# Performance work log

Measured on AMD Instinct MI355X. Metric: run time of the kernel, lower is better.

## Reference

```python
import jax, jax.numpy as jnp
import numpy as np

B, N, E = 16, 10000, 160000
C_IN, C_SP, C_OUT = 32, 16, 32


def _glorot(key, shape):
    s = float(np.sqrt(6.0 / (shape[0] + shape[1])))
    return jax.random.uniform(key, shape, jnp.float32, -s, s)


def setup_inputs() -> dict:
    key = jax.random.key(0)
    ks = jax.random.split(key, 12)
    X = jax.random.normal(ks[0], (B, N, C_IN), jnp.float32)
    edge_index1 = jax.random.randint(ks[1], (2, E), 0, N)
    edge_weight1 = jax.random.uniform(ks[2], (E,), jnp.float32)
    res_n_id1 = jnp.arange(N)
    edge_index2 = jax.random.randint(ks[3], (2, E), 0, N)
    edge_weight2 = jax.random.uniform(ks[4], (E,), jnp.float32)
    res_n_id2 = jnp.arange(N)
    # conv1 params (in=C_IN, out=C_SP, edge_channels=1, concat=True)
    amp_w1 = _glorot(ks[5], (1, C_IN))            # [edge_ch, in]
    gate_w1 = _glorot(ks[6], (2 * C_IN + 1, 1))   # Linear(2*in+edge_ch, 1)
    gate_b1 = jnp.zeros((1,), jnp.float32)
    w1 = _glorot(ks[7], (2 * C_IN, C_SP))         # concat weight
    b1 = jnp.zeros((C_SP,), jnp.float32)
    # conv2 params (in=C_SP, out=C_OUT)
    amp_w2 = _glorot(ks[8], (1, C_SP))
    gate_w2 = _glorot(ks[9], (2 * C_SP + 1, 1))
    gate_b2 = jnp.zeros((1,), jnp.float32)
    w2 = _glorot(ks[10], (2 * C_SP, C_OUT))
    b2 = jnp.zeros((C_OUT,), jnp.float32)
    return dict(X=X, edge_index1=edge_index1, edge_weight1=edge_weight1, res_n_id1=res_n_id1,
                edge_index2=edge_index2, edge_weight2=edge_weight2, res_n_id2=res_n_id2,
                amp_w1=amp_w1, gate_w1=gate_w1, gate_b1=gate_b1, w1=w1, b1=b1,
                amp_w2=amp_w2, gate_w2=gate_w2, gate_b2=gate_b2, w2=w2, b2=b2)


def _sagela(x_src, x_dst, edge_index, edge_weight, amp_w, gate_w, gate_b, w, b):
    # x_src: [B, N_src, C], x_dst: [B, N_dst, C]
    src, dst = edge_index[0], edge_index[1]
    n_dst = x_dst.shape[1]
    C = x_src.shape[-1]
    x_j = x_src[:, src]                       # [B, E, C] gathered source feats
    x_i = x_dst[:, dst]                       # [B, E, C] gathered target feats
    e = edge_weight[:, None]                  # [E, 1] edge features
    # gate_linear(cat[x_i, x_j, e]) split into three matmuls (same math)
    wg_i, wg_j, wg_e = gate_w[:C], gate_w[C:2 * C], gate_w[2 * C:]
    lamb = jax.nn.sigmoid(x_i @ wg_i + x_j @ wg_j + (e @ wg_e)[None] + gate_b)  # [B, E, 1]
    amp = e @ amp_w                           # [E, C] edge amplification
    msg = amp[None, :, :] * x_j * lamb        # [B, E, C]
    # mean aggregation over incoming edges (scatter-add / count)
    aggr = jnp.zeros((x_src.shape[0], n_dst, C), msg.dtype).at[:, dst].add(msg)
    cnt = jnp.zeros((n_dst,), msg.dtype).at[dst].add(1.0)
    aggr = aggr / jnp.maximum(cnt, 1.0)[None, :, None]
    out = jnp.concatenate([x_dst, aggr], axis=-1) @ w + b  # [B, N_dst, out]
    return out


def reference(X, edge_index1, edge_weight1, res_n_id1, edge_index2, edge_weight2, res_n_id2,
              amp_w1, gate_w1, gate_b1, w1, b1, amp_w2, gate_w2, gate_b2, w2, b2):
    h = _sagela(X, X[:, res_n_id1], edge_index1, edge_weight1, amp_w1, gate_w1, gate_b1, w1, b1)
    h = jax.nn.leaky_relu(h, 0.01)
    out = _sagela(h, h[:, res_n_id2], edge_index2, edge_weight2, amp_w2, gate_w2, gate_b2, w2, b2)
    return out
```

## Files before the change

kernel.cpp:

```cpp
#include <hip/hip_runtime.h>
#include <math.h>

#define B 16
#define N 10000
#define E 160000
#define CAP 64

__device__ __forceinline__ ushort f2bf(float v) {
    uint u = __float_as_uint(v);
    u = (u + 0x7fffu + ((u >> 16) & 1u)) >> 16;
    return (ushort)u;
}
__device__ __forceinline__ float bf2f(ushort u) { return __uint_as_float(((uint)u) << 16); }
__device__ __forceinline__ float bf2f_lo(uint u) { return __uint_as_float(u << 16); }
__device__ __forceinline__ float bf2f_hi(uint u) { return __uint_as_float(u & 0xffff0000u); }
__device__ __forceinline__ float dec_ew(uint u) {
    return ((float)(u >> 14) + 0.5f) * (1.0f / 262144.0f);
}

__global__ __launch_bounds__(256, 8)
void prep_fused_kernel(const float* __restrict__ X,
                       const float* __restrict__ gate_w1,
                       const float* __restrict__ amp_w1,
                       const float* __restrict__ b1,
                       const int* __restrict__ ei1, const float* __restrict__ ew1,
                       const int* __restrict__ ei2, const float* __restrict__ ew2,
                       const float* __restrict__ w1,
                       ushort* __restrict__ yt,
                       float* __restrict__ xpart,
                       float* __restrict__ gi, float* __restrict__ gj,
                       int* __restrict__ bcount1, uint* __restrict__ bucket1,
                       int* __restrict__ bcount2, uint* __restrict__ bucket2) {
    __shared__ __align__(16) float s_w1[64 * 16];
    __shared__ float s_x[16][33];
    __shared__ float s_py[16][17];

    int tid = threadIdx.x;
    int gtid = blockIdx.x * 256 + tid;

    if (gtid < 2 * E) {
        if (gtid < E) {
            int t = gtid;
            int d = ei1[E + t];
            int pos = atomicAdd(&bcount1[d], 1);
            if (pos < CAP) {
                uint q = (uint)(ew1[t] * 262144.0f);
                if (q > 262143u) q = 262143u;
                bucket1[d * CAP + pos] = (q << 14) | (uint)ei1[t];
            }
        } else {
            int e = gtid - E;
            int d = ei2[E + e];
            int pos = atomicAdd(&bcount2[d], 1);
            if (pos < CAP) {
                uint q = (uint)(ew2[e] * 262144.0f);
                if (q > 262143u) q = 262143u;
                bucket2[d * CAP + pos] = (q << 14) | (uint)ei2[e];
            }
        }
    }

    {
        int i = tid * 4;
        *(float4*)&s_w1[i] = *(const float4*)&w1[i];
    }
    int b = tid >> 4, o = tid & 15;
    for (int n = blockIdx.x; n < N; n += gridDim.x) {
        __syncthreads();
        {
            int bb = tid >> 4, c2 = (tid & 15) * 2;
            float2 v = *(const float2*)(X + ((size_t)bb * N + n) * 32 + c2);
            s_x[bb][c2] = v.x; s_x[bb][c2 + 1] = v.y;
        }
        __syncthreads();

        float po = b1[o], py = 0.f;
        #pragma unroll
        for (int c = 0; c < 32; ++c) {
            float xa = s_x[b][c];
            po += xa * s_w1[c * 16 + o];
            py += amp_w1[c] * xa * s_w1[(32 + c) * 16 + o];
        }
        float pi = s_x[b][o] * gate_w1[o]      + s_x[b][o + 16] * gate_w1[o + 16];
        float pj = s_x[b][o] * gate_w1[32 + o] + s_x[b][o + 16] * gate_w1[48 + o];
        #pragma unroll
        for (int off = 8; off; off >>= 1) {
            pi += __shfl_xor(pi, off, 16);
            pj += __shfl_xor(pj, off, 16);
        }
        int r = n * 16 + b;
        xpart[(size_t)r * 16 + o] = po;
        s_py[b][o] = py;
        if (o == 0) { gi[r] = pi; gj[r] = pj; }
        __syncthreads();

        if (tid < 64) {
            int bb = tid >> 2, j = tid & 3;
            uint lo = (uint)f2bf(s_py[bb][4 * j])     | ((uint)f2bf(s_py[bb][4 * j + 1]) << 16);
            uint hi = (uint)f2bf(s_py[bb][4 * j + 2]) | ((uint)f2bf(s_py[bb][4 * j + 3]) << 16);
            ((uint2*)yt)[(size_t)(n * 16 + bb) * 4 + j] = make_uint2(lo, hi);
        }
    }
}

__global__ __launch_bounds__(256, 8)
void agg1_kernel(const uint4* __restrict__ y4,
                 const float* __restrict__ xpart,
                 const float* __restrict__ gi,
                 const float* __restrict__ gj,
                 const int* __restrict__ bcount,
                 const uint* __restrict__ bucket,
                 const float* __restrict__ gate_w,
                 const float* __restrict__ gate_b,
                 const float* __restrict__ gate_w2,
                 ushort* __restrict__ htb,
                 float* __restrict__ gi2, float* __restrict__ gj2) {
    int tid = threadIdx.x;
    int wv = tid >> 6, l = tid & 63;
    int n = blockIdx.x * 4 + wv;
    int og = l & 1, b = (l >> 1) & 15, h = l >> 5;

    int cnt = bcount[n];
    int deg = cnt < CAP ? cnt : CAP;
    float wge = gate_w[64];
    float gib = gi[n * 16 + b] + gate_b[0];
    const uint* __restrict__ eb = bucket + (size_t)n * CAP;

    float a0 = 0.f, a1 = 0.f, a2 = 0.f, a3 = 0.f;
    float a4 = 0.f, a5 = 0.f, a6 = 0.f, a7 = 0.f;
    for (int k = h; k < deg; k += 2) {
        uint pr = eb[k];
        uint src = pr & 0x3FFFu;
        float w = dec_ew(pr);
        float z = gib + gj[src * 16 + b] + w * wge;
        float cc = w / (1.0f + __expf(-z));
        uint4 u = y4[src * 32u + (uint)b * 2u + og];
        a0 += cc * bf2f_lo(u.x); a1 += cc * bf2f_hi(u.x);
        a2 += cc * bf2f_lo(u.y); a3 += cc * bf2f_hi(u.y);
        a4 += cc * bf2f_lo(u.z); a5 += cc * bf2f_hi(u.z);
        a6 += cc * bf2f_lo(u.w); a7 += cc * bf2f_hi(u.w);
    }
    a0 += __shfl_xor(a0, 32, 64); a1 += __shfl_xor(a1, 32, 64);
    a2 += __shfl_xor(a2, 32, 64); a3 += __shfl_xor(a3, 32, 64);
    a4 += __shfl_xor(a4, 32, 64); a5 += __shfl_xor(a5, 32, 64);
    a6 += __shfl_xor(a6, 32, 64); a7 += __shfl_xor(a7, 32, 64);

    if (h == 0) {
        float inv = 1.0f / fmaxf((float)cnt, 1.0f);
        size_t xb = ((size_t)n * 16 + b) * 16 + 8 * og;
        float4 xp0 = *(const float4*)&xpart[xb];
        float4 xp1 = *(const float4*)&xpart[xb + 4];
        float v0 = xp0.x + inv * a0, v1 = xp0.y + inv * a1;
        float v2 = xp0.z + inv * a2, v3 = xp0.w + inv * a3;
        float v4 = xp1.x + inv * a4, v5 = xp1.y + inv * a5;
        float v6 = xp1.z + inv * a6, v7 = xp1.w + inv * a7;
        v0 = v0 > 0.f ? v0 : 0.01f * v0;  v1 = v1 > 0.f ? v1 : 0.01f * v1;
        v2 = v2 > 0.f ? v2 : 0.01f * v2;  v3 = v3 > 0.f ? v3 : 0.01f * v3;
        v4 = v4 > 0.f ? v4 : 0.01f * v4;  v5 = v5 > 0.f ? v5 : 0.01f * v5;
        v6 = v6 > 0.f ? v6 : 0.01f * v6;  v7 = v7 > 0.f ? v7 : 0.01f * v7;
        uint4 pk;
        pk.x = (uint)f2bf(v0) | ((uint)f2bf(v1) << 16);
        pk.y = (uint)f2bf(v2) | ((uint)f2bf(v3) << 16);
        pk.z = (uint)f2bf(v4) | ((uint)f2bf(v5) << 16);
        pk.w = (uint)f2bf(v6) | ((uint)f2bf(v7) << 16);
        ((uint4*)htb)[(size_t)n * 32 + b * 2 + og] = pk;
        int ob = 8 * og;
        float pi = v0 * gate_w2[ob]     + v1 * gate_w2[ob + 1]
                 + v2 * gate_w2[ob + 2] + v3 * gate_w2[ob + 3]
                 + v4 * gate_w2[ob + 4] + v5 * gate_w2[ob + 5]
                 + v6 * gate_w2[ob + 6] + v7 * gate_w2[ob + 7];
        float pj = v0 * gate_w2[16 + ob]     + v1 * gate_w2[16 + ob + 1]
                 + v2 * gate_w2[16 + ob + 2] + v3 * gate_w2[16 + ob + 3]
                 + v4 * gate_w2[16 + ob + 4] + v5 * gate_w2[16 + ob + 5]
                 + v6 * gate_w2[16 + ob + 6] + v7 * gate_w2[16 + ob + 7];
        pi += __shfl_xor(pi, 1, 64);
        pj += __shfl_xor(pj, 1, 64);
        if (og == 0) { gi2[n * 16 + b] = pi; gj2[n * 16 + b] = pj; }
    }
}

__global__ __launch_bounds__(256, 8)
void agg2_kernel(const uint4* __restrict__ htb4,
                 const float* __restrict__ gi,
                 const float* __restrict__ gj,
                 const int* __restrict__ bcount,
                 const uint* __restrict__ bucket,
                 const float* __restrict__ gate_w,
                 const float* __restrict__ gate_b,
                 const float* __restrict__ amp_w,
                 const float* __restrict__ w2,
                 const float* __restrict__ b2,
                 float* __restrict__ out) {
    __shared__ __align__(16) float s_w2[32 * 36];
    __shared__ __align__(16) float s_in[4][16][36];

    int tid = threadIdx.x;
    int n0 = blockIdx.x * 4;

    {
        int kk = tid >> 3, o4g = tid & 7;
        *(float4*)&s_w2[kk * 36 + 4 * o4g] = *(const float4*)&w2[kk * 32 + 4 * o4g];
    }
    if (tid < 128) {
        int nl = tid >> 5, idx = tid & 31;
        uint4 u = htb4[(size_t)(n0 + nl) * 32 + idx];
        int b = idx >> 1, cb = (idx & 1) * 8;
        float4 f0, f1;
        f0.x = bf2f_lo(u.x); f0.y = bf2f_hi(u.x);
        f0.z = bf2f_lo(u.y); f0.w = bf2f_hi(u.y);
        f1.x = bf2f_lo(u.z); f1.y = bf2f_hi(u.z);
        f1.z = bf2f_lo(u.w); f1.w = bf2f_hi(u.w);
        *(float4*)&s_in[nl][b][cb]     = f0;
        *(float4*)&s_in[nl][b][cb + 4] = f1;
    }
    __syncthreads();

    int wv = tid >> 6, l = tid & 63;
    int n = n0 + wv;
    int og = l & 1, b = (l >> 1) & 15, h = l >> 5;
    int cnt = bcount[n];
    int deg = cnt < CAP ? cnt : CAP;
    float wge = gate_w[32];
    float gib = gi[n * 16 + b] + gate_b[0];
    const uint* __restrict__ eb = bucket + (size_t)n * CAP;

    float a0 = 0.f, a1 = 0.f, a2 = 0.f, a3 = 0.f;
    float a4 = 0.f, a5 = 0.f, a6 = 0.f, a7 = 0.f;
    for (int k = h; k < deg; k += 2) {
        uint pr = eb[k];
        uint src = pr & 0x3FFFu;
        float w = dec_ew(pr);
        float z = gib + gj[src * 16 + b] + w * wge;
        float cc = w / (1.0f + __expf(-z));
        uint4 u = htb4[src * 32u + (uint)b * 2u + og];
        a0 += cc * bf2f_lo(u.x); a1 += cc * bf2f_hi(u.x);
        a2 += cc * bf2f_lo(u.y); a3 += cc * bf2f_hi(u.y);
        a4 += cc * bf2f_lo(u.z); a5 += cc * bf2f_hi(u.z);
        a6 += cc * bf2f_lo(u.w); a7 += cc * bf2f_hi(u.w);
    }
    a0 += __shfl_xor(a0, 32, 64); a1 += __shfl_xor(a1, 32, 64);
    a2 += __shfl_xor(a2, 32, 64); a3 += __shfl_xor(a3, 32, 64);
    a4 += __shfl_xor(a4, 32, 64); a5 += __shfl_xor(a5, 32, 64);
    a6 += __shfl_xor(a6, 32, 64); a7 += __shfl_xor(a7, 32, 64);
    if (h == 0) {
        float inv = 1.0f / fmaxf((float)cnt, 1.0f);
        int cb = 8 * og;
        float4 f0, f1;
        f0.x = a0 * amp_w[cb]     * inv;  f0.y = a1 * amp_w[cb + 1] * inv;
        f0.z = a2 * amp_w[cb + 2] * inv;  f0.w = a3 * amp_w[cb + 3] * inv;
        f1.x = a4 * amp_w[cb + 4] * inv;  f1.y = a5 * amp_w[cb + 5] * inv;
        f1.z = a6 * amp_w[cb + 6] * inv;  f1.w = a7 * amp_w[cb + 7] * inv;
        *(float4*)&s_in[wv][b][16 + cb]     = f0;
        *(float4*)&s_in[wv][b][16 + cb + 4] = f1;
    }
    __syncthreads();

    {
        int o4 = tid & 7, bb = (tid >> 3) & 15, half = tid >> 7;
        int nlA = half * 2, nlB = half * 2 + 1;
        float4 bias = *(const float4*)&b2[4 * o4];
        float4 acc0 = bias, acc1 = bias;
        #pragma unroll
        for (int k4 = 0; k4 < 8; ++k4) {
            float4 ivA = *(const float4*)&s_in[nlA][bb][4 * k4];
            float4 ivB = *(const float4*)&s_in[nlB][bb][4 * k4];
            float4 w0 = *(const float4*)&s_w2[(4 * k4)     * 36 + 4 * o4];
            float4 w1 = *(const float4*)&s_w2[(4 * k4 + 1) * 36 + 4 * o4];
            float4 wv2 = *(const float4*)&s_w2[(4 * k4 + 2) * 36 + 4 * o4];
            float4 w3 = *(const float4*)&s_w2[(4 * k4 + 3) * 36 + 4 * o4];
            acc0.x += ivA.x * w0.x + ivA.y * w1.x + ivA.z * wv2.x + ivA.w * w3.x;
            acc0.y += ivA.x * w0.y + ivA.y * w1.y + ivA.z * wv2.y + ivA.w * w3.y;
            acc0.z += ivA.x * w0.z + ivA.y * w1.z + ivA.z * wv2.z + ivA.w * w3.z;
            acc0.w += ivA.x * w0.w + ivA.y * w1.w + ivA.z * wv2.w + ivA.w * w3.w;
            acc1.x += ivB.x * w0.x + ivB.y * w1.x + ivB.z * wv2.x + ivB.w * w3.x;
            acc1.y += ivB.x * w0.y + ivB.y * w1.y + ivB.z * wv2.y + ivB.w * w3.y;
            acc1.z += ivB.x * w0.z + ivB.y * w1.z + ivB.z * wv2.z + ivB.w * w3.z;
            acc1.w += ivB.x * w0.w + ivB.y * w1.w + ivB.z * wv2.w + ivB.w * w3.w;
        }
        *(float4*)(out + ((size_t)bb * N + (n0 + nlA)) * 32 + 4 * o4) = acc0;
        *(float4*)(out + ((size_t)bb * N + (n0 + nlB)) * 32 + 4 * o4) = acc1;
    }
}

extern "C" void kernel_launch(void* const* d_in, const int* in_sizes, int n_in,
                              void* d_out, int out_size, void* d_ws, size_t ws_size,
                              hipStream_t stream) {
    const float* X       = (const float*)d_in[0];
    const int*   ei1     = (const int*)  d_in[1];
    const float* ew1     = (const float*)d_in[2];
    const int*   ei2     = (const int*)  d_in[4];
    const float* ew2     = (const float*)d_in[5];
    const float* amp_w1  = (const float*)d_in[7];
    const float* gate_w1 = (const float*)d_in[8];
    const float* gate_b1 = (const float*)d_in[9];
    const float* w1      = (const float*)d_in[10];
    const float* b1      = (const float*)d_in[11];
    const float* amp_w2  = (const float*)d_in[12];
    const float* gate_w2 = (const float*)d_in[13];
    const float* gate_b2 = (const float*)d_in[14];
    const float* w2      = (const float*)d_in[15];
    const float* b2      = (const float*)d_in[16];
    float* out = (float*)d_out;

    char* p = (char*)d_ws;
    ushort* yt     = (ushort*)p; p += (size_t)N * B * 16 * sizeof(ushort);
    ushort* htb    = (ushort*)p; p += (size_t)N * B * 16 * sizeof(ushort);
    float* xpart   = (float*)p;  p += (size_t)N * B * 16 * sizeof(float);
    float* gi1     = (float*)p;  p += (size_t)N * B * sizeof(float);
    float* gj1     = (float*)p;  p += (size_t)N * B * sizeof(float);
    float* gi2     = (float*)p;  p += (size_t)N * B * sizeof(float);
    float* gj2     = (float*)p;  p += (size_t)N * B * sizeof(float);
    uint*  bucket1 = (uint*)p;   p += (size_t)N * CAP * sizeof(uint);
    uint*  bucket2 = (uint*)p;   p += (size_t)N * CAP * sizeof(uint);
    int*   bcount1 = (int*)p;    p += (size_t)N * sizeof(int);
    int*   bcount2 = (int*)p;    p += (size_t)N * sizeof(int);

    hipMemsetAsync(bcount1, 0, 2 * (size_t)N * sizeof(int), stream);
    prep_fused_kernel<<<2048, 256, 0, stream>>>(
        X, gate_w1, amp_w1, b1, ei1, ew1, ei2, ew2, w1,
        yt, xpart, gi1, gj1,
        bcount1, bucket1, bcount2, bucket2);

    agg1_kernel<<<N / 4, 256, 0, stream>>>(
        (const uint4*)yt, xpart, gi1, gj1, bcount1, bucket1,
        gate_w1, gate_b1, gate_w2, htb, gi2, gj2);

    agg2_kernel<<<N / 4, 256, 0, stream>>>(
        (const uint4*)htb, gi2, gj2, bcount2, bucket2,
        gate_w2, gate_b2, amp_w2, w2, b2, out);
}
```

Before: 207.5 us.

## Preload edge buckets per lane, unroll gather by two, split agg2 over batch halves

Both aggregation kernels now load the node's 64 bucket entries once, one per lane, and broadcast them with shuffles instead of re-reading them from global memory. The gather loop handles two edges per iteration so two independent gathers are in flight at once. agg2 launches twice as many blocks, each covering half the batch, with four lanes splitting the edge list and a two-step shuffle reduction. This is meant to raise memory-level parallelism and occupancy, at the cost of more shuffles, extra predication, and repeated per-block setup such as loading w2 into shared memory.

Measured after the change: 173.0 us. 1.2x faster.

```diff
diff --git a/kernel.cpp b/kernel.cpp
--- a/kernel.cpp
+++ b/kernel.cpp
@@ -124,21 +124,31 @@
     int deg = cnt < CAP ? cnt : CAP;
     float wge = gate_w[64];
     float gib = gi[n * 16 + b] + gate_b[0];
-    const uint* __restrict__ eb = bucket + (size_t)n * CAP;
+    uint my_pr = bucket[(size_t)n * CAP + l];
 
     float a0 = 0.f, a1 = 0.f, a2 = 0.f, a3 = 0.f;
     float a4 = 0.f, a5 = 0.f, a6 = 0.f, a7 = 0.f;
-    for (int k = h; k < deg; k += 2) {
-        uint pr = eb[k];
-        uint src = pr & 0x3FFFu;
-        float w = dec_ew(pr);
-        float z = gib + gj[src * 16 + b] + w * wge;
-        float cc = w / (1.0f + __expf(-z));
-        uint4 u = y4[src * 32u + (uint)b * 2u + og];
-        a0 += cc * bf2f_lo(u.x); a1 += cc * bf2f_hi(u.x);
-        a2 += cc * bf2f_lo(u.y); a3 += cc * bf2f_hi(u.y);
-        a4 += cc * bf2f_lo(u.z); a5 += cc * bf2f_hi(u.z);
-        a6 += cc * bf2f_lo(u.w); a7 += cc * bf2f_hi(u.w);
+    for (int k = h; k < deg; k += 4) {
+        int k1 = k + 2;
+        bool v1 = k1 < deg;
+        uint pr0 = __shfl(my_pr, k, 64);
+        uint pr1 = __shfl(my_pr, v1 ? k1 : k, 64);
+        uint s0 = pr0 & 0x3FFFu, s1 = pr1 & 0x3FFFu;
+        float g0 = gj[s0 * 16 + b];
+        float g1 = gj[s1 * 16 + b];
+        uint4 u0 = y4[s0 * 32u + (uint)b * 2u + og];
+        uint4 u1 = y4[s1 * 32u + (uint)b * 2u + og];
+        float w0 = dec_ew(pr0), w1 = dec_ew(pr1);
+        float c0 = w0 / (1.0f + __expf(-(gib + g0 + w0 * wge)));
+        float c1 = v1 ? (w1 / (1.0f + __expf(-(gib + g1 + w1 * wge)))) : 0.f;
+        a0 += c0 * bf2f_lo(u0.x) + c1 * bf2f_lo(u1.x);
+        a1 += c0 * bf2f_hi(u0.x) + c1 * bf2f_hi(u1.x);
+        a2 += c0 * bf2f_lo(u0.y) + c1 * bf2f_lo(u1.y);
+        a3 += c0 * bf2f_hi(u0.y) + c1 * bf2f_hi(u1.y);
+        a4 += c0 * bf2f_lo(u0.z) + c1 * bf2f_lo(u1.z);
+        a5 += c0 * bf2f_hi(u0.z) + c1 * bf2f_hi(u1.z);
+        a6 += c0 * bf2f_lo(u0.w) + c1 * bf2f_lo(u1.w);
+        a7 += c0 * bf2f_hi(u0.w) + c1 * bf2f_hi(u1.w);
     }
     a0 += __shfl_xor(a0, 32, 64); a1 += __shfl_xor(a1, 32, 64);
     a2 += __shfl_xor(a2, 32, 64); a3 += __shfl_xor(a3, 32, 64);
@@ -192,57 +202,74 @@
                  const float* __restrict__ b2,
                  float* __restrict__ out) {
     __shared__ __align__(16) float s_w2[32 * 36];
-    __shared__ __align__(16) float s_in[4][16][36];
+    __shared__ __align__(16) float s_in[4][8][36];
 
     int tid = threadIdx.x;
-    int n0 = blockIdx.x * 4;
+    const int nb = N / 4;
+    int bg = blockIdx.x / nb;
+    int n0 = (blockIdx.x - bg * nb) * 4;
 
     {
         int kk = tid >> 3, o4g = tid & 7;
         *(float4*)&s_w2[kk * 36 + 4 * o4g] = *(const float4*)&w2[kk * 32 + 4 * o4g];
     }
-    if (tid < 128) {
-        int nl = tid >> 5, idx = tid & 31;
-        uint4 u = htb4[(size_t)(n0 + nl) * 32 + idx];
-        int b = idx >> 1, cb = (idx & 1) * 8;
+    if (tid < 64) {
+        int nl = tid >> 4, idx = tid & 15;
+        uint4 u = htb4[(size_t)(n0 + nl) * 32 + bg * 16 + idx];
+        int bl = idx >> 1, cb = (idx & 1) * 8;
         float4 f0, f1;
         f0.x = bf2f_lo(u.x); f0.y = bf2f_hi(u.x);
         f0.z = bf2f_lo(u.y); f0.w = bf2f_hi(u.y);
         f1.x = bf2f_lo(u.z); f1.y = bf2f_hi(u.z);
         f1.z = bf2f_lo(u.w); f1.w = bf2f_hi(u.w);
-        *(float4*)&s_in[nl][b][cb]     = f0;
-        *(float4*)&s_in[nl][b][cb + 4] = f1;
+        *(float4*)&s_in[nl][bl][cb]     = f0;
+        *(float4*)&s_in[nl][bl][cb + 4] = f1;
     }
     __syncthreads();
 
     int wv = tid >> 6, l = tid & 63;
     int n = n0 + wv;
-    int og = l & 1, b = (l >> 1) & 15, h = l >> 5;
+    int og = l & 1, bl = (l >> 1) & 7, q = l >> 4;
+    int b = bg * 8 + bl;
     int cnt = bcount[n];
     int deg = cnt < CAP ? cnt : CAP;
     float wge = gate_w[32];
     float gib = gi[n * 16 + b] + gate_b[0];
-    const uint* __restrict__ eb = bucket + (size_t)n * CAP;
+    uint my_pr = bucket[(size_t)n * CAP + l];
 
     float a0 = 0.f, a1 = 0.f, a2 = 0.f, a3 = 0.f;
     float a4 = 0.f, a5 = 0.f, a6 = 0.f, a7 = 0.f;
-    for (int k = h; k < deg; k += 2) {
-        uint pr = eb[k];
-        uint src = pr & 0x3FFFu;
-        float w = dec_ew(pr);
-        float z = gib + gj[src * 16 + b] + w * wge;
-        float cc = w / (1.0f + __expf(-z));
-        uint4 u = htb4[src * 32u + (uint)b * 2u + og];
-        a0 += cc * bf2f_lo(u.x); a1 += cc * bf2f_hi(u.x);
-        a2 += cc * bf2f_lo(u.y); a3 += cc * bf2f_hi(u.y);
-        a4 += cc * bf2f_lo(u.z); a5 += cc * bf2f_hi(u.z);
-        a6 += cc * bf2f_lo(u.w); a7 += cc * bf2f_hi(u.w);
-    }
-    a0 += __shfl_xor(a0, 32, 64); a1 += __shfl_xor(a1, 32, 64);
-    a2 += __shfl_xor(a2, 32, 64); a3 += __shfl_xor(a3, 32, 64);
-    a4 += __shfl_xor(a4, 32, 64); a5 += __shfl_xor(a5, 32, 64);
-    a6 += __shfl_xor(a6, 32, 64); a7 += __shfl_xor(a7, 32, 64);
-    if (h == 0) {
+    for (int k = q; k < deg; k += 8) {
+        int k1 = k + 4;
+        bool v1 = k1 < deg;
+        uint pr0 = __shfl(my_pr, k, 64);
+        uint pr1 = __shfl(my_pr, v1 ? k1 : k, 64);
+        uint s0 = pr0 & 0x3FFFu, s1 = pr1 & 0x3FFFu;
+        float g0 = gj[s0 * 16 + b];
+        float g1 = gj[s1 * 16 + b];
+        uint4 u0 = htb4[s0 * 32u + (uint)b * 2u + og];
+        uint4 u1 = htb4[s1 * 32u + (uint)b * 2u + og];
+        float w0 = dec_ew(pr0), w1 = dec_ew(pr1);
+        float c0 = w0 / (1.0f + __expf(-(gib + g0 + w0 * wge)));
+        float c1 = v1 ? (w1 / (1.0f + __expf(-(gib + g1 + w1 * wge)))) : 0.f;
+        a0 += c0 * bf2f_lo(u0.x) + c1 * bf2f_lo(u1.x);
+        a1 += c0 * bf2f_hi(u0.x) + c1 * bf2f_hi(u1.x);
+        a2 += c0 * bf2f_lo(u0.y) + c1 * bf2f_lo(u1.y);
+        a3 += c0 * bf2f_hi(u0.y) + c1 * bf2f_hi(u1.y);
+        a4 += c0 * bf2f_lo(u0.z) + c1 * bf2f_lo(u1.z);
+        a5 += c0 * bf2f_hi(u0.z) + c1 * bf2f_hi(u1.z);
+        a6 += c0 * bf2f_lo(u0.w) + c1 * bf2f_lo(u1.w);
+        a7 += c0 * bf2f_hi(u0.w) + c1 * bf2f_hi(u1.w);
+    }
+    a0 += __shfl_xor(a0, 16, 64); a0 += __shfl_xor(a0, 32, 64);
+    a1 += __shfl_xor(a1, 16, 64); a1 += __shfl_xor(a1, 32, 64);
+    a2 += __shfl_xor(a2, 16, 64); a2 += __shfl_xor(a2, 32, 64);
+    a3 += __shfl_xor(a3, 16, 64); a3 += __shfl_xor(a3, 32, 64);
+    a4 += __shfl_xor(a4, 16, 64); a4 += __shfl_xor(a4, 32, 64);
+    a5 += __shfl_xor(a5, 16, 64); a5 += __shfl_xor(a5, 32, 64);
+    a6 += __shfl_xor(a6, 16, 64); a6 += __shfl_xor(a6, 32, 64);
+    a7 += __shfl_xor(a7, 16, 64); a7 += __shfl_xor(a7, 32, 64);
+    if (q == 0) {
         float inv = 1.0f / fmaxf((float)cnt, 1.0f);
         int cb = 8 * og;
         float4 f0, f1;
@@ -250,35 +277,28 @@
         f0.z = a2 * amp_w[cb + 2] * inv;  f0.w = a3 * amp_w[cb + 3] * inv;
         f1.x = a4 * amp_w[cb + 4] * inv;  f1.y = a5 * amp_w[cb + 5] * inv;
         f1.z = a6 * amp_w[cb + 6] * inv;  f1.w = a7 * amp_w[cb + 7] * inv;
-        *(float4*)&s_in[wv][b][16 + cb]     = f0;
-        *(float4*)&s_in[wv][b][16 + cb + 4] = f1;
+        *(float4*)&s_in[wv][bl][16 + cb]     = f0;
+        *(float4*)&s_in[wv][bl][16 + cb + 4] = f1;
     }
     __syncthreads();
 
     {
-        int o4 = tid & 7, bb = (tid >> 3) & 15, half = tid >> 7;
-        int nlA = half * 2, nlB = half * 2 + 1;
-        float4 bias = *(const float4*)&b2[4 * o4];
-        float4 acc0 = bias, acc1 = bias;
+        int o4 = tid & 7, bl2 = (tid >> 3) & 7, nl = tid >> 6;
+        float4 acc = *(const float4*)&b2[4 * o4];
         #pragma unroll
         for (int k4 = 0; k4 < 8; ++k4) {
-            float4 ivA = *(const float4*)&s_in[nlA][bb][4 * k4];
-            float4 ivB = *(const float4*)&s_in[nlB][bb][4 * k4];
+            float4 iv = *(const float4*)&s_in[nl][bl2][4 * k4];
             float4 w0 = *(const float4*)&s_w2[(4 * k4)     * 36 + 4 * o4];
             float4 w1 = *(const float4*)&s_w2[(4 * k4 + 1) * 36 + 4 * o4];
             float4 wv2 = *(const float4*)&s_w2[(4 * k4 + 2) * 36 + 4 * o4];
             float4 w3 = *(const float4*)&s_w2[(4 * k4 + 3) * 36 + 4 * o4];
-            acc0.x += ivA.x * w0.x + ivA.y * w1.x + ivA.z * wv2.x + ivA.w * w3.x;
-            acc0.y += ivA.x * w0.y + ivA.y * w1.y + ivA.z * wv2.y + ivA.w * w3.y;
-            acc0.z += ivA.x * w0.z + ivA.y * w1.z + ivA.z * wv2.z + ivA.w * w3.z;
-            acc0.w += ivA.x * w0.w + ivA.y * w1.w + ivA.z * wv2.w + ivA.w * w3.w;
-            acc1.x += ivB.x * w0.x + ivB.y * w1.x + ivB.z * wv2.x + ivB.w * w3.x;
-            acc1.y += ivB.x * w0.y + ivB.y * w1.y + ivB.z * wv2.y + ivB.w * w3.y;
-            acc1.z += ivB.x * w0.z + ivB.y * w1.z + ivB.z * wv2.z + ivB.w * w3.z;
-            acc1.w += ivB.x * w0.w + ivB.y * w1.w + ivB.z * wv2.w + ivB.w * w3.w;
-        }
-        *(float4*)(out + ((size_t)bb * N + (n0 + nlA)) * 32 + 4 * o4) = acc0;
-        *(float4*)(out + ((size_t)bb * N + (n0 + nlB)) * 32 + 4 * o4) = acc1;
+            acc.x += iv.x * w0.x + iv.y * w1.x + iv.z * wv2.x + iv.w * w3.x;
+            acc.y += iv.x * w0.y + iv.y * w1.y + iv.z * wv2.y + iv.w * w3.y;
+            acc.z += iv.x * w0.z + iv.y * w1.z + iv.z * wv2.z + iv.w * w3.z;
+            acc.w += iv.x * w0.w + iv.y * w1.w + iv.z * wv2.w + iv.w * w3.w;
+        }
+        size_t ob = ((size_t)(bg * 8 + bl2) * N + (n0 + nl)) * 32;
+        *(float4*)(out + ob + 4 * o4) = acc;
     }
 }
 
@@ -325,7 +345,7 @@
         (const uint4*)yt, xpart, gi1, gj1, bcount1, bucket1,
         gate_w1, gate_b1, gate_w2, htb, gi2, gj2);
 
-    agg2_kernel<<<N / 4, 256, 0, stream>>>(
+    agg2_kernel<<<2 * (N / 4), 256, 0, stream>>>(
         (const uint4*)htb, gi2, gj2, bcount2, bucket2,
         gate_w2, gate_b2, amp_w2, w2, b2, out);
 }
```
